# Optimization experiments

Hardware: AMD Instinct MI355X
Metric: run time of the kernel (lower is better)

Reference implementation:

```python
import jax, jax.numpy as jnp
import numpy as np

H = 1024       # hidden_dim
NH = 16        # num_attention_heads
HD = H // NH   # head_dim = 64
ROT = 32       # rotary_dim
MP = 8         # MP_NUM hardcoded in forward
NEG_INF = jnp.float32(-1e9)


def setup_inputs() -> dict:
    key = jax.random.key(0)
    k1, k2, k3 = jax.random.split(key, 3)
    hidden_states = jax.random.normal(k1, (2, 2048, H), dtype=jnp.float32)
    w_qkv = jax.random.normal(k2, (H, 3 * H), dtype=jnp.float32) * 0.02
    w_out = jax.random.normal(k3, (H, H), dtype=jnp.float32) * 0.02
    return {"hidden_states": hidden_states, "w_qkv": w_qkv, "w_out": w_out}


def _rotate_every_two(x):
    # GPT-J rotate: (x0,x1,x2,x3,...) -> (-x1,x0,-x3,x2,...)
    x1 = x[..., ::2]
    x2 = x[..., 1::2]
    return jnp.stack((-x2, x1), axis=-1).reshape(x.shape)


def _apply_rope(x, sin, cos):
    return x * cos + _rotate_every_two(x) * sin


def reference(hidden_states, w_qkv, w_out):
    B, S, _ = hidden_states.shape
    qkv = hidden_states @ w_qkv                      # [B,S,3H]
    qkv = qkv.reshape(B, S, MP, 3 * H // MP)         # GPT-J MP-split layout
    local = NH * HD // MP
    q = qkv[..., :local]
    k = qkv[..., local:2 * local]
    v = qkv[..., 2 * local:]

    def split_heads(x):  # [B,S,MP,H/MP] -> [B,S,NH,HD]
        return x.reshape(B, S, MP, NH // MP, HD).reshape(B, S, NH, HD)

    q, k, v = split_heads(q), split_heads(k), split_heads(v)

    # fixed position embedding (GPT-J), offset=0, seq dim = 1
    inv_freq = 1.0 / (10000.0 ** (jnp.arange(0, ROT, 2, dtype=jnp.float32) / ROT))
    sinusoid = jnp.einsum('i,j->ij', jnp.arange(S, dtype=jnp.float32), inv_freq)  # [S,ROT/2]
    sin = jnp.repeat(jnp.sin(sinusoid), 2, axis=-1)[None, :, None, :]             # [1,S,1,ROT]
    cos = jnp.repeat(jnp.cos(sinusoid), 2, axis=-1)[None, :, None, :]

    q = jnp.concatenate([_apply_rope(q[..., :ROT], sin, cos), q[..., ROT:]], axis=-1)
    k = jnp.concatenate([_apply_rope(k[..., :ROT], sin, cos), k[..., ROT:]], axis=-1)

    q = q.transpose(0, 2, 1, 3)  # [B,NH,S,HD]
    k = k.transpose(0, 2, 1, 3)
    v = v.transpose(0, 2, 1, 3)

    # manual causal attention in fp32 (as the torch code casts q,k to fp32)
    scores = jnp.einsum('bhqd,bhkd->bhqk', q, k) / jnp.sqrt(jnp.float32(HD))
    causal = jnp.tril(jnp.ones((S, S), dtype=bool))[None, None]
    scores = jnp.where(causal, scores, NEG_INF)
    probs = jax.nn.softmax(scores, axis=-1)
    attn = jnp.einsum('bhqk,bhkd->bhqd', probs, v)   # [B,NH,S,HD]

    attn = attn.transpose(0, 2, 1, 3).reshape(B, S, H)  # merge heads
    return attn @ w_out
```

## Files before the change

### kernel.cpp

```cpp
#include <hip/hip_runtime.h>

#define SEQ   2048
#define NHEADS 16
#define HDIM  64
#define HID   1024
#define ROT   32

typedef __attribute__((ext_vector_type(8))) short  short8;
typedef __attribute__((ext_vector_type(4))) float  floatx4;

__device__ __forceinline__ ushort f2bf(float f) {
    union { float f; uint u; } v; v.f = f;
    uint x = v.u;
    uint r = (x + 0x7FFFu + ((x >> 16) & 1u)) >> 16;
    return (ushort)r;
}

__device__ __forceinline__ float fexp2(float x) {
    return __builtin_amdgcn_exp2f(x);
}

__device__ __forceinline__ floatx4 mfma_bf16(short8 a, short8 b, floatx4 c) {
    return __builtin_amdgcn_mfma_f32_16x16x32_bf16(a, b, c, 0, 0, 0);
}

__device__ __forceinline__ void gload16(const ushort* g, ushort* l) {
    __builtin_amdgcn_global_load_lds(
        (const __attribute__((address_space(1))) void*)g,
        (__attribute__((address_space(3))) void*)l, 16, 0, 0);
}

__global__ __launch_bounds__(256) void convert_bf16_kernel(
    const float* __restrict__ src, ushort* __restrict__ dst, int n)
{
    int i = (blockIdx.x * 256 + threadIdx.x) * 8;
    if (i >= n) return;
    float4 a = *(const float4*)(src + i);
    float4 b = *(const float4*)(src + i + 4);
    short8 v;
    v[0] = (short)f2bf(a.x); v[1] = (short)f2bf(a.y);
    v[2] = (short)f2bf(a.z); v[3] = (short)f2bf(a.w);
    v[4] = (short)f2bf(b.x); v[5] = (short)f2bf(b.y);
    v[6] = (short)f2bf(b.z); v[7] = (short)f2bf(b.w);
    *(short8*)(dst + i) = v;
}

__global__ __launch_bounds__(256) void transpose_bf16_kernel(
    const float* __restrict__ src, ushort* __restrict__ dst, int K, int N)
{
    __shared__ ushort Tl[64 * 68];
    const int k0 = blockIdx.y * 64, n0 = blockIdx.x * 64;
    const int tid = threadIdx.x;
    #pragma unroll
    for (int i = 0; i < 4; i++) {
        int lin = tid + 256 * i;
        int row = lin >> 4;
        int c4  = (lin & 15) * 4;
        float4 v = *(const float4*)(src + (size_t)(k0 + row) * N + n0 + c4);
        uint2 u;
        u.x = (uint)f2bf(v.x) | ((uint)f2bf(v.y) << 16);
        u.y = (uint)f2bf(v.z) | ((uint)f2bf(v.w) << 16);
        *(uint2*)&Tl[row * 68 + c4] = u;
    }
    __syncthreads();
    #pragma unroll
    for (int j = 0; j < 2; j++) {
        int lin = tid + 256 * j;
        int n = lin >> 3, c = lin & 7;
        short8 v;
        #pragma unroll
        for (int u = 0; u < 8; u++) v[u] = (short)Tl[(c * 8 + u) * 68 + n];
        *(short8*)(dst + (size_t)(n0 + n) * K + k0 + c * 8) = v;
    }
}

__global__ __launch_bounds__(256) void qkv_rope_kernel(
    const ushort* __restrict__ hbf,
    const ushort* __restrict__ wqkvT,
    ushort* __restrict__ Qb, ushort* __restrict__ Kb, ushort* __restrict__ Vb)
{
    __shared__ ushort Al[2][128 * 32];
    __shared__ ushort Bl[2][128 * 32];
    const int tid  = threadIdx.x;
    const int lane = tid & 63;
    const int wv   = tid >> 6;
    const int g    = lane >> 4;
    const int l15  = lane & 15;

    const int lin  = blockIdx.x + 24 * blockIdx.y;
    const int xcd  = lin & 7;
    const int slot = lin >> 3;
    const int cxi  = xcd & 1, cyi = xcd >> 1;
    const int sx   = slot % 12, sy = slot / 12;
    const int n0   = (cxi * 12 + sx) * 128;
    const int m0   = (cyi * 8 + sy) * 128;

    const int wr = (wv >> 1) * 64;
    const int wc = (wv & 1) * 64;
    const int rowl = lane >> 2;
    const int kcol = (lane & 3) * 8;

    floatx4 acc[4][4];
    #pragma unroll
    for (int a = 0; a < 4; a++)
        #pragma unroll
        for (int bq = 0; bq < 4; bq++)
            acc[a][bq] = floatx4{0.f, 0.f, 0.f, 0.f};

    const ushort* ga = hbf   + (size_t)(m0 + wv * 32 + rowl) * 1024 + kcol;
    const ushort* gb = wqkvT + (size_t)(n0 + wv * 32 + rowl) * 1024 + kcol;
    const int lofs = wv * 1024;

    gload16(ga,             &Al[0][lofs]);
    gload16(ga + 16 * 1024, &Al[0][lofs + 512]);
    gload16(gb,             &Bl[0][lofs]);
    gload16(gb + 16 * 1024, &Bl[0][lofs + 512]);
    asm volatile("s_waitcnt vmcnt(0)" ::: "memory");
    __builtin_amdgcn_s_barrier();

    for (int it = 0; it < 32; it++) {
        const int cur = it & 1;
        if (it + 1 < 32) {
            const int k0 = (it + 1) * 32;
            const int nxt = cur ^ 1;
            gload16(ga + k0,             &Al[nxt][lofs]);
            gload16(ga + k0 + 16 * 1024, &Al[nxt][lofs + 512]);
            gload16(gb + k0,             &Bl[nxt][lofs]);
            gload16(gb + k0 + 16 * 1024, &Bl[nxt][lofs + 512]);
        }
        short8 af[4], bfr[4];
        #pragma unroll
        for (int fm = 0; fm < 4; fm++)
            af[fm] = *(const short8*)&Al[cur][(wr + fm * 16 + l15) * 32 + g * 8];
        #pragma unroll
        for (int fn = 0; fn < 4; fn++)
            bfr[fn] = *(const short8*)&Bl[cur][(wc + fn * 16 + l15) * 32 + g * 8];
        #pragma unroll
        for (int fm = 0; fm < 4; fm++)
            #pragma unroll
            for (int fn = 0; fn < 4; fn++)
                acc[fm][fn] = mfma_bf16(af[fm], bfr[fn], acc[fm][fn]);
        asm volatile("s_waitcnt vmcnt(0)" ::: "memory");
        __builtin_amdgcn_s_barrier();
    }

    #pragma unroll
    for (int fn = 0; fn < 4; fn++) {
        const int c    = n0 + wc + fn * 16 + l15;
        const int mp   = c / 384;
        const int rem  = c - mp * 384;
        const int tsel = rem >> 7;
        const int j    = (rem >> 6) & 1;
        const int d    = rem & 63;
        const int head = mp * 2 + j;
        ushort* basep = (tsel == 0) ? Qb : (tsel == 1) ? Kb : Vb;
        const bool rope = (tsel < 2) && (d < ROT);
        const float qscale = (tsel == 0) ? 0.18033688011112042f : 1.0f;
        float freq = 0.f;
        if (rope) {
            freq = exp2f((float)(d >> 1) * -0.830482023721841f);
        }
        #pragma unroll
        for (int fm = 0; fm < 4; fm++) {
            #pragma unroll
            for (int r = 0; r < 4; r++) {
                int row = m0 + wr + fm * 16 + g * 4 + r;
                int bb  = row >> 11;
                int s   = row & 2047;
                float val = acc[fm][fn][r];
                float pv  = __shfl_xor(val, 1, 64);
                float outv = val;
                if (rope) {
                    float ang = (float)s * freq;
                    float sn, cs;
                    __sincosf(ang, &sn, &cs);
                    outv = ((d & 1) == 0) ? (val * cs - pv * sn)
                                          : (val * cs + pv * sn);
                }
                outv *= qscale;
                size_t off;
                if (tsel == 2)
                    off = ((size_t)(bb * NHEADS + head) * HDIM + d) * SEQ + s;
                else
                    off = ((size_t)(bb * NHEADS + head) * SEQ + s) * HDIM + d;
                basep[off] = f2bf(outv);
            }
        }
    }
}

__global__ __launch_bounds__(512, 4) void attn_kernel(
    const ushort* __restrict__ Qb, const ushort* __restrict__ Kb,
    const ushort* __restrict__ Vb, ushort* __restrict__ attn)
{
    __shared__ ushort Kl[2][64 * 72];
    __shared__ ushort Vt[2][64 * 72];

    const int tid  = threadIdx.x;
    const int lane = tid & 63;
    const int wv   = tid >> 6;
    const int g    = lane >> 4;
    const int l15  = lane & 15;

    const int l    = blockIdx.x + 16 * blockIdx.y + 256 * blockIdx.z;
    const int half = l >> 8;
    const int xx   = l & 15;
    const int hh   = (l >> 4) & 15;
    const int qb   = half ? xx : 15 - xx;
    const int bb   = half;

    const int q0 = qb * 128;
    const int wq = wv * 16;
    const size_t kvbase = (size_t)(bb * NHEADS + hh) * SEQ * HDIM;

    const int srow = tid >> 3;
    const int sch  = (tid & 7) * 8;

    short8 qreg[2];
    #pragma unroll
    for (int ks = 0; ks < 2; ks++)
        qreg[ks] = *(const short8*)(Qb + kvbase +
            (size_t)(q0 + wq + l15) * HDIM + ks * 32 + g * 8);

    float m = -__builtin_inff();
    float lsum = 0.f;
    floatx4 of[4];
    #pragma unroll
    for (int df = 0; df < 4; df++) of[df] = floatx4{0.f, 0.f, 0.f, 0.f};

    const int nt = 2 * qb + 2;

    auto load_tile = [&](int tt, short8& kr, short8& vr) {
        const int kv = tt * 64;
        kr = *(const short8*)(Kb + kvbase + (size_t)(kv + srow) * HDIM + sch);
        vr = *(const short8*)(Vb + kvbase + (size_t)srow * SEQ + kv + sch);
    };
    auto write_tile = [&](int buf, short8& kr, short8& vr) {
        *(short8*)&Kl[buf][srow * 72 + sch] = kr;
        *(short8*)&Vt[buf][srow * 72 + sch] = vr;
    };
    auto compute_tile = [&](int t, const ushort* Kc, const ushort* Vc) {
        const int kv0 = t * 64;
        if (kv0 > q0 + wq + 15) return;
        floatx4 sf[4];
        __builtin_amdgcn_s_setprio(1);
        #pragma unroll
        for (int kf = 0; kf < 4; kf++) {
            short8 kr0 = *(const short8*)&Kc[(kf * 16 + l15) * 72 + g * 8];
            short8 kr1 = *(const short8*)&Kc[(kf * 16 + l15) * 72 + 32 + g * 8];
            floatx4 s = floatx4{0.f, 0.f, 0.f, 0.f};
            s = mfma_bf16(kr0, qreg[0], s);
            s = mfma_bf16(kr1, qreg[1], s);
            sf[kf] = s;
        }
        __builtin_amdgcn_s_setprio(0);

        const bool diag = (kv0 + 63 > q0 + wq);
        const int qg = q0 + wq + l15;
        float tmax = -__builtin_inff();
        if (diag) {
            #pragma unroll
            for (int kf = 0; kf < 4; kf++) {
                #pragma unroll
                for (int r = 0; r < 4; r++) {
                    int key = kv0 + kf * 16 + g * 4 + r;
                    float x = sf[kf][r];
                    if (key > qg) x = -1e9f;
                    sf[kf][r] = x;
                    tmax = fmaxf(tmax, x);
                }
            }
        } else {
            #pragma unroll
            for (int kf = 0; kf < 4; kf++)
                #pragma unroll
                for (int r = 0; r < 4; r++)
                    tmax = fmaxf(tmax, sf[kf][r]);
        }
        if (!__all(tmax <= m + 8.0f)) {
            tmax = fmaxf(tmax, __shfl_xor(tmax, 16, 64));
            tmax = fmaxf(tmax, __shfl_xor(tmax, 32, 64));
            float mn = fmaxf(m, tmax);
            float f  = fexp2(m - mn);
            m = mn;
            lsum *= f;
            #pragma unroll
            for (int r = 0; r < 4; r++) {
                float fr = __shfl(f, g * 4 + r, 64);
                #pragma unroll
                for (int df = 0; df < 4; df++)
                    of[df][r] *= fr;
            }
        }
        float rs = 0.f;
        #pragma unroll
        for (int kf = 0; kf < 4; kf++) {
            #pragma unroll
            for (int r = 0; r < 4; r++) {
                float p = fexp2(sf[kf][r] - m);
                sf[kf][r] = p;
                rs += p;
            }
        }
        lsum += rs;
        short8 pa[2];
        #pragma unroll
        for (int ks = 0; ks < 2; ks++) {
            union { short8 s; uint u[4]; } pu;
            #pragma unroll
            for (int w = 0; w < 4; w++) {
                const int kf = 2 * ks + (w >> 1);
                float lo = sf[kf][(w & 1) * 2 + 0];
                float hi = sf[kf][(w & 1) * 2 + 1];
                asm("v_cvt_pk_bf16_f32 %0, %1, %2"
                    : "=v"(pu.u[w]) : "v"(lo), "v"(hi));
            }
            pa[ks] = pu.s;
        }
        __builtin_amdgcn_s_setprio(1);
        #pragma unroll
        for (int df = 0; df < 4; df++) {
            #pragma unroll
            for (int ks = 0; ks < 2; ks++) {
                const int vb = (df * 16 + l15) * 72 + ks * 32 + g * 4;
                uint2 v0 = *(const uint2*)&Vc[vb];
                uint2 v1 = *(const uint2*)&Vc[vb + 16];
                union { short8 s; uint4 u; } vv;
                vv.u.x = v0.x; vv.u.y = v0.y; vv.u.z = v1.x; vv.u.w = v1.y;
                of[df] = mfma_bf16(pa[ks], vv.s, of[df]);
            }
        }
        __builtin_amdgcn_s_setprio(0);
    };

    short8 kA, vA, kB, vB;
    load_tile(0, kA, vA);
    if (nt > 1) load_tile(1, kB, vB);
    write_tile(0, kA, vA);
    __syncthreads();

    for (int t = 0; t < nt; t += 2) {
        if (t + 2 < nt) load_tile(t + 2, kA, vA);
        compute_tile(t, Kl[0], Vt[0]);
        write_tile(1, kB, vB);
        __syncthreads();
        if (t + 3 < nt) load_tile(t + 3, kB, vB);
        compute_tile(t + 1, Kl[1], Vt[1]);
        if (t + 2 < nt) write_tile(0, kA, vA);
        __syncthreads();
    }

    lsum += __shfl_xor(lsum, 16, 64);
    lsum += __shfl_xor(lsum, 32, 64);
    #pragma unroll
    for (int r = 0; r < 4; r++) {
        float lr = __shfl(lsum, g * 4 + r, 64);
        float inv = 1.0f / lr;
        int q = q0 + wq + g * 4 + r;
        #pragma unroll
        for (int df = 0; df < 4; df++)
            attn[((size_t)bb * SEQ + q) * HID + hh * 64 + df * 16 + l15] =
                f2bf(of[df][r] * inv);
    }
}

__global__ __launch_bounds__(256) void out_proj_kernel(
    const ushort* __restrict__ attn,
    const ushort* __restrict__ woutT,
    float* __restrict__ out)
{
    __shared__ ushort Al[2][128 * 32];
    __shared__ ushort Bl[2][128 * 32];
    const int tid  = threadIdx.x;
    const int lane = tid & 63;
    const int wv   = tid >> 6;
    const int g    = lane >> 4;
    const int l15  = lane & 15;

    const int lin  = blockIdx.x + 8 * blockIdx.y;
    const int xcd  = lin & 7;
    const int slot = lin >> 3;
    const int cxi  = xcd & 1, cyi = xcd >> 1;
    const int sx   = slot & 3, sy = slot >> 2;
    const int n0   = (cxi * 4 + sx) * 128;
    const int m0   = (cyi * 8 + sy) * 128;

    const int wr = (wv >> 1) * 64;
    const int wc = (wv & 1) * 64;
    const int rowl = lane >> 2;
    const int kcol = (lane & 3) * 8;

    floatx4 acc[4][4];
    #pragma unroll
    for (int a = 0; a < 4; a++)
        #pragma unroll
        for (int bq = 0; bq < 4; bq++)
            acc[a][bq] = floatx4{0.f, 0.f, 0.f, 0.f};

    const ushort* ga = attn  + (size_t)(m0 + wv * 32 + rowl) * 1024 + kcol;
    const ushort* gb = woutT + (size_t)(n0 + wv * 32 + rowl) * 1024 + kcol;
    const int lofs = wv * 1024;

    gload16(ga,             &Al[0][lofs]);
    gload16(ga + 16 * 1024, &Al[0][lofs + 512]);
    gload16(gb,             &Bl[0][lofs]);
    gload16(gb + 16 * 1024, &Bl[0][lofs + 512]);
    asm volatile("s_waitcnt vmcnt(0)" ::: "memory");
    __builtin_amdgcn_s_barrier();

    for (int it = 0; it < 32; it++) {
        const int cur = it & 1;
        if (it + 1 < 32) {
            const int k0 = (it + 1) * 32;
            const int nxt = cur ^ 1;
            gload16(ga + k0,             &Al[nxt][lofs]);
            gload16(ga + k0 + 16 * 1024, &Al[nxt][lofs + 512]);
            gload16(gb + k0,             &Bl[nxt][lofs]);
            gload16(gb + k0 + 16 * 1024, &Bl[nxt][lofs + 512]);
        }
        short8 af[4], bfr[4];
        #pragma unroll
        for (int fm = 0; fm < 4; fm++)
            af[fm] = *(const short8*)&Al[cur][(wr + fm * 16 + l15) * 32 + g * 8];
        #pragma unroll
        for (int fn = 0; fn < 4; fn++)
            bfr[fn] = *(const short8*)&Bl[cur][(wc + fn * 16 + l15) * 32 + g * 8];
        #pragma unroll
        for (int fm = 0; fm < 4; fm++)
            #pragma unroll
            for (int fn = 0; fn < 4; fn++)
                acc[fm][fn] = mfma_bf16(af[fm], bfr[fn], acc[fm][fn]);
        asm volatile("s_waitcnt vmcnt(0)" ::: "memory");
        __builtin_amdgcn_s_barrier();
    }
    #pragma unroll
    for (int fm = 0; fm < 4; fm++)
        #pragma unroll
        for (int fn = 0; fn < 4; fn++)
            #pragma unroll
            for (int r = 0; r < 4; r++) {
                int row = m0 + wr + fm * 16 + g * 4 + r;
                int col = n0 + wc + fn * 16 + l15;
                out[(size_t)row * 1024 + col] = acc[fm][fn][r];
            }
}

extern "C" void kernel_launch(void* const* d_in, const int* in_sizes, int n_in,
                              void* d_out, int out_size, void* d_ws, size_t ws_size,
                              hipStream_t stream)
{
    const float* hidden = (const float*)d_in[0];
    const float* wqkv   = (const float*)d_in[1];
    const float* wout   = (const float*)d_in[2];
    float* out = (float*)d_out;

    const size_t NELEM = (size_t)2 * SEQ * HID;
    ushort* Qb    = (ushort*)d_ws;
    ushort* Kb    = Qb + NELEM;
    ushort* Vb    = Kb + NELEM;
    ushort* hbf   = Vb + NELEM;
    ushort* wqkvT = hbf + NELEM;
    ushort* woutT = wqkvT + (size_t)3072 * 1024;
    ushort* attnb = hbf;

    convert_bf16_kernel<<<2048, 256, 0, stream>>>(hidden, hbf, (int)NELEM);
    transpose_bf16_kernel<<<dim3(48, 16), 256, 0, stream>>>(wqkv, wqkvT, 1024, 3072);
    transpose_bf16_kernel<<<dim3(16, 16), 256, 0, stream>>>(wout, woutT, 1024, 1024);
    qkv_rope_kernel<<<dim3(24, 32), 256, 0, stream>>>(hbf, wqkvT, Qb, Kb, Vb);
    attn_kernel<<<dim3(16, NHEADS, 2), 512, 0, stream>>>(Qb, Kb, Vb, attnb);
    out_proj_kernel<<<dim3(8, 32), 256, 0, stream>>>(attnb, woutT, out);
}
```

Baseline: 129.9 us.

## Triple-buffer LDS staging in QKV and output projection GEMMs

Both projection GEMM kernels move from double to triple buffering in LDS. Tiles are prefetched two k-steps ahead, and each step waits with vmcnt(4) instead of draining all outstanding loads, so more global-load latency is hidden behind MFMA work. LDS use per block grows by half (48KB), which may reduce occupancy. The attention kernel, which likely dominates runtime, is unchanged.

Result: slower. 152.0 us (+17.0%).

```diff
diff --git a/kernel.cpp b/kernel.cpp
--- a/kernel.cpp
+++ b/kernel.cpp
@@ -79,8 +79,8 @@
     const ushort* __restrict__ wqkvT,
     ushort* __restrict__ Qb, ushort* __restrict__ Kb, ushort* __restrict__ Vb)
 {
-    __shared__ ushort Al[2][128 * 32];
-    __shared__ ushort Bl[2][128 * 32];
+    __shared__ ushort Al[3 * 4096];
+    __shared__ ushort Bl[3 * 4096];
     const int tid  = threadIdx.x;
     const int lane = tid & 63;
     const int wv   = tid >> 6;
@@ -111,37 +111,39 @@
     const ushort* gb = wqkvT + (size_t)(n0 + wv * 32 + rowl) * 1024 + kcol;
     const int lofs = wv * 1024;
 
-    gload16(ga,             &Al[0][lofs]);
-    gload16(ga + 16 * 1024, &Al[0][lofs + 512]);
-    gload16(gb,             &Bl[0][lofs]);
-    gload16(gb + 16 * 1024, &Bl[0][lofs + 512]);
-    asm volatile("s_waitcnt vmcnt(0)" ::: "memory");
+    auto stage = [&](int t, int obuf) {
+        const int k0 = t * 32;
+        gload16(ga + k0,             &Al[obuf + lofs]);
+        gload16(ga + k0 + 16 * 1024, &Al[obuf + lofs + 512]);
+        gload16(gb + k0,             &Bl[obuf + lofs]);
+        gload16(gb + k0 + 16 * 1024, &Bl[obuf + lofs + 512]);
+    };
+
+    int o0 = 0, o1 = 4096, o2 = 8192;
+    stage(0, o0);
+    stage(1, o1);
+    asm volatile("s_waitcnt vmcnt(4)" ::: "memory");
     __builtin_amdgcn_s_barrier();
 
     for (int it = 0; it < 32; it++) {
-        const int cur = it & 1;
-        if (it + 1 < 32) {
-            const int k0 = (it + 1) * 32;
-            const int nxt = cur ^ 1;
-            gload16(ga + k0,             &Al[nxt][lofs]);
-            gload16(ga + k0 + 16 * 1024, &Al[nxt][lofs + 512]);
-            gload16(gb + k0,             &Bl[nxt][lofs]);
-            gload16(gb + k0 + 16 * 1024, &Bl[nxt][lofs + 512]);
-        }
+        const bool pre = (it + 2 < 32);
+        if (pre) stage(it + 2, o2);
         short8 af[4], bfr[4];
         #pragma unroll
         for (int fm = 0; fm < 4; fm++)
-            af[fm] = *(const short8*)&Al[cur][(wr + fm * 16 + l15) * 32 + g * 8];
+            af[fm] = *(const short8*)&Al[o0 + (wr + fm * 16 + l15) * 32 + g * 8];
         #pragma unroll
         for (int fn = 0; fn < 4; fn++)
-            bfr[fn] = *(const short8*)&Bl[cur][(wc + fn * 16 + l15) * 32 + g * 8];
+            bfr[fn] = *(const short8*)&Bl[o0 + (wc + fn * 16 + l15) * 32 + g * 8];
         #pragma unroll
         for (int fm = 0; fm < 4; fm++)
             #pragma unroll
             for (int fn = 0; fn < 4; fn++)
                 acc[fm][fn] = mfma_bf16(af[fm], bfr[fn], acc[fm][fn]);
-        asm volatile("s_waitcnt vmcnt(0)" ::: "memory");
+        if (pre) asm volatile("s_waitcnt vmcnt(4)" ::: "memory");
+        else     asm volatile("s_waitcnt vmcnt(0)" ::: "memory");
         __builtin_amdgcn_s_barrier();
+        int tmp = o0; o0 = o1; o1 = o2; o2 = tmp;
     }
 
     #pragma unroll
@@ -369,8 +371,8 @@
     const ushort* __restrict__ woutT,
     float* __restrict__ out)
 {
-    __shared__ ushort Al[2][128 * 32];
-    __shared__ ushort Bl[2][128 * 32];
+    __shared__ ushort Al[3 * 4096];
+    __shared__ ushort Bl[3 * 4096];
     const int tid  = threadIdx.x;
     const int lane = tid & 63;
     const int wv   = tid >> 6;
@@ -401,37 +403,39 @@
     const ushort* gb = woutT + (size_t)(n0 + wv * 32 + rowl) * 1024 + kcol;
     const int lofs = wv * 1024;
 
-    gload16(ga,             &Al[0][lofs]);
-    gload16(ga + 16 * 1024, &Al[0][lofs + 512]);
-    gload16(gb,             &Bl[0][lofs]);
-    gload16(gb + 16 * 1024, &Bl[0][lofs + 512]);
-    asm volatile("s_waitcnt vmcnt(0)" ::: "memory");
+    auto stage = [&](int t, int obuf) {
+        const int k0 = t * 32;
+        gload16(ga + k0,             &Al[obuf + lofs]);
+        gload16(ga + k0 + 16 * 1024, &Al[obuf + lofs + 512]);
+        gload16(gb + k0,             &Bl[obuf + lofs]);
+        gload16(gb + k0 + 16 * 1024, &Bl[obuf + lofs + 512]);
+    };
+
+    int o0 = 0, o1 = 4096, o2 = 8192;
+    stage(0, o0);
+    stage(1, o1);
+    asm volatile("s_waitcnt vmcnt(4)" ::: "memory");
     __builtin_amdgcn_s_barrier();
 
     for (int it = 0; it < 32; it++) {
-        const int cur = it & 1;
-        if (it + 1 < 32) {
-            const int k0 = (it + 1) * 32;
-            const int nxt = cur ^ 1;
-            gload16(ga + k0,             &Al[nxt][lofs]);
-            gload16(ga + k0 + 16 * 1024, &Al[nxt][lofs + 512]);
-            gload16(gb + k0,             &Bl[nxt][lofs]);
-            gload16(gb + k0 + 16 * 1024, &Bl[nxt][lofs + 512]);
-        }
+        const bool pre = (it + 2 < 32);
+        if (pre) stage(it + 2, o2);
         short8 af[4], bfr[4];
         #pragma unroll
         for (int fm = 0; fm < 4; fm++)
-            af[fm] = *(const short8*)&Al[cur][(wr + fm * 16 + l15) * 32 + g * 8];
+            af[fm] = *(const short8*)&Al[o0 + (wr + fm * 16 + l15) * 32 + g * 8];
         #pragma unroll
         for (int fn = 0; fn < 4; fn++)
-            bfr[fn] = *(const short8*)&Bl[cur][(wc + fn * 16 + l15) * 32 + g * 8];
+            bfr[fn] = *(const short8*)&Bl[o0 + (wc + fn * 16 + l15) * 32 + g * 8];
         #pragma unroll
         for (int fm = 0; fm < 4; fm++)
             #pragma unroll
             for (int fn = 0; fn < 4; fn++)
                 acc[fm][fn] = mfma_bf16(af[fm], bfr[fn], acc[fm][fn]);
-        asm volatile("s_waitcnt vmcnt(0)" ::: "memory");
+        if (pre) asm volatile("s_waitcnt vmcnt(4)" ::: "memory");
+        else     asm volatile("s_waitcnt vmcnt(0)" ::: "memory");
         __builtin_amdgcn_s_barrier();
+        int tmp = o0; o0 = o1; o1 = o2; o2 = tmp;
     }
     #pragma unroll
     for (int fm = 0; fm < 4; fm++)
```
